# Performance work log

Hardware: AMD Instinct MI355X
Metric: run time of the kernel (lower is better)

The kernel has to match this reference:

```python
import jax, jax.numpy as jnp
import numpy as np

UNITS = 1024      # LSTM hidden size
FEAT = 128        # num_features (Dense output == cell input for feedback)
T = 48            # warmup sequence length
B = 2048          # batch
OUT_STEPS = 24
S0, S1 = 0, 128   # output_indices[0] : output_indices[-1]+1


def setup_inputs() -> dict:
    key = jax.random.key(0)
    k0, k1, k2, k3 = jax.random.split(key, 4)
    inputs = jax.random.normal(k0, (B, T, FEAT), dtype=jnp.float32)
    # Keras LSTMCell params: kernel [F,4U], recurrent_kernel [U,4U], bias [4U] (gate order i,f,c,o)
    kernel = jax.random.normal(k1, (FEAT, 4 * UNITS), dtype=jnp.float32) * 0.05
    recurrent_kernel = jax.random.normal(k2, (UNITS, 4 * UNITS), dtype=jnp.float32) * 0.02
    bias = jnp.zeros((4 * UNITS,), dtype=jnp.float32)
    dense_w = jax.random.normal(k3, (UNITS, FEAT), dtype=jnp.float32) * 0.03
    dense_b = jnp.zeros((FEAT,), dtype=jnp.float32)
    return {"inputs": inputs, "kernel": kernel, "recurrent_kernel": recurrent_kernel,
            "bias": bias, "dense_w": dense_w, "dense_b": dense_b}


def _lstm_step(h, c, x, kernel, recurrent_kernel, bias):
    # Keras LSTMCell: z = x@W + h@U + b, gates split as (i, f, g, o)
    z = x @ kernel + h @ recurrent_kernel + bias
    i, f, g, o = jnp.split(z, 4, axis=-1)
    i = jax.nn.sigmoid(i)
    f = jax.nn.sigmoid(f)
    g = jnp.tanh(g)
    o = jax.nn.sigmoid(o)
    c_new = f * c + i * g
    h_new = o * jnp.tanh(c_new)
    return h_new, c_new


def reference(inputs, kernel, recurrent_kernel, bias, dense_w, dense_b):
    bsz = inputs.shape[0]
    h0 = jnp.zeros((bsz, UNITS), dtype=inputs.dtype)
    c0 = jnp.zeros((bsz, UNITS), dtype=inputs.dtype)

    # warmup: RNN over the input sequence, keep final state
    def warm_step(carry, x_t):
        h, c = carry
        h, c = _lstm_step(h, c, x_t, kernel, recurrent_kernel, bias)
        return (h, c), None

    (h, c), _ = jax.lax.scan(warm_step, (h0, c0), jnp.swapaxes(inputs, 0, 1))  # xs: [T,B,F]
    y = h @ dense_w + dense_b  # first prediction, [B, F]

    def dec_step(carry, _):
        h, c, y_prev = carry
        h, c = _lstm_step(h, c, y_prev, kernel, recurrent_kernel, bias)
        y_new = h @ dense_w + dense_b
        return (h, c, y_new), y_new[:, S0:S1]

    _, ys_rest = jax.lax.scan(dec_step, (h, c, y), None, length=OUT_STEPS - 1)  # [OUT-1,B,S]
    ys = jnp.concatenate([y[None, :, S0:S1], ys_rest], axis=0)  # [OUT,B,S]
    return jnp.transpose(ys, (1, 0, 2))  # [B, OUT, S]
```

## Files before the change

kernel.cpp:

```cpp
#include <hip/hip_runtime.h>
#include <math.h>

#define UNITS 1024
#define FEAT 128
#define TSEQ 48
#define BATCH 2048
#define OUT_STEPS 24
#define KTOT 1152
#define N4 4096

typedef unsigned short ushort;
typedef __attribute__((ext_vector_type(8))) short bf16x8;
typedef __attribute__((ext_vector_type(4))) float f32x4;

__device__ __forceinline__ ushort f2bf(float f) {
  unsigned u = __float_as_uint(f);
  unsigned r = (u + 0x7FFF + ((u >> 16) & 1)) >> 16;
  return (ushort)r;
}
__device__ __forceinline__ float sigm(float x) { return 1.0f / (1.0f + __expf(-x)); }
__device__ __forceinline__ float tanh_f(float x) { return 1.0f - 2.0f / (1.0f + __expf(2.0f * x)); }

__device__ __forceinline__ void gload_lds16(const void* g, void* l) {
  __builtin_amdgcn_global_load_lds(
      (const __attribute__((address_space(1))) unsigned int*)g,
      (__attribute__((address_space(3))) unsigned int*)l, 16, 0, 0);
}


__global__ __launch_bounds__(256)
void convert_inputs_kernel(const float* __restrict__ in, ushort* __restrict__ Xb) {
  const int o4 = (blockIdx.x * 256 + threadIdx.x) * 4;
  const int t = o4 >> 18;
  const int b = (o4 >> 7) & 2047;
  const int f = o4 & 127;
  const float4 v = *reinterpret_cast<const float4*>(&in[(size_t)(b * TSEQ + t) * FEAT + f]);
  union { ushort u[4]; unsigned long long ll; } w;
  w.u[0] = f2bf(v.x); w.u[1] = f2bf(v.y); w.u[2] = f2bf(v.z); w.u[3] = f2bf(v.w);
  *reinterpret_cast<unsigned long long*>(&Xb[o4]) = w.ll;
}

__global__ __launch_bounds__(256)
void prep_w_kernel(const float* __restrict__ kW, const float* __restrict__ rW,
                   ushort* __restrict__ Wp) {
  __shared__ ushort tile[32][65];
  const int t = threadIdx.x;
  const int k0 = blockIdx.x * 32;
  const int n0 = blockIdx.y * 64;
#pragma unroll
  for (int p = 0; p < 8; ++p) {
    const int li = p * 256 + t;
    const int nn = li & 63, kk = li >> 6;
    const int np = n0 + nn;
    const int u16 = np & 15, gg = (np >> 4) & 3, ugrp = np >> 6;
    const int nsrc = gg * 1024 + ugrp * 16 + u16;
    const int k = k0 + kk;
    const float v = (k < FEAT) ? kW[(size_t)k * N4 + nsrc] : rW[(size_t)(k - FEAT) * N4 + nsrc];
    tile[kk][nn] = f2bf(v);
  }
  __syncthreads();
#pragma unroll
  for (int p = 0; p < 8; ++p) {
    const int li = p * 256 + t;
    const int kk = li & 31, nn = li >> 5;
    Wp[(size_t)(n0 + nn) * KTOT + k0 + kk] = tile[kk][nn];
  }
}

__global__ __launch_bounds__(256)
void prep_wd_kernel(const float* __restrict__ dw, ushort* __restrict__ Wdt) {
  const int o = blockIdx.x * 256 + threadIdx.x;
  const int n = o >> 10, k = o & 1023;
  Wdt[o] = f2bf(dw[(size_t)k * FEAT + n]);
}

__global__ __launch_bounds__(256)
void prep_b2_kernel(const float* __restrict__ bias, const float* __restrict__ db,
                    const float* __restrict__ W, float* __restrict__ b2) {
  const int n = blockIdx.x * 256 + threadIdx.x;
  float s = bias[n];
#pragma unroll 8
  for (int f = 0; f < FEAT; ++f) s += db[f] * W[(size_t)f * N4 + n];
  b2[n] = s;
}

__global__ __launch_bounds__(256)
void prep_u_kernel(const float* __restrict__ dw,
                   const float* __restrict__ W,
                   const float* __restrict__ rW,
                   ushort* __restrict__ Wp2) {
  __shared__ float sWd[64][132];
  __shared__ float sW[128][68];
  const int tid = threadIdx.x;
  const int ugrp = blockIdx.x;
  const int k0 = blockIdx.y * 64;
  const int n0 = ugrp * 64;

#pragma unroll
  for (int p = 0; p < 8; ++p) {
    const int li = p * 256 + tid;
    const int kk = li >> 5, f4 = (li & 31) * 4;
    *reinterpret_cast<float4*>(&sWd[kk][f4]) =
        *reinterpret_cast<const float4*>(&dw[(size_t)(k0 + kk) * FEAT + f4]);
  }
#pragma unroll
  for (int p = 0; p < 32; ++p) {
    const int li = p * 256 + tid;
    const int f = li >> 6, nn = li & 63;
    const int u16 = nn & 15, gg = (nn >> 4) & 3;
    const int nsrc = gg * 1024 + ugrp * 16 + u16;
    sW[f][nn] = W[(size_t)f * N4 + nsrc];
  }
  __syncthreads();

  const int tx = tid & 15;
  const int ty = tid >> 4;
  float acc[4][4] = {};
  for (int f = 0; f < 128; ++f) {
    float a[4], b[4];
#pragma unroll
    for (int j = 0; j < 4; ++j) a[j] = sWd[tx * 4 + j][f];
#pragma unroll
    for (int i = 0; i < 4; ++i) b[i] = sW[f][ty * 4 + i];
#pragma unroll
    for (int i = 0; i < 4; ++i)
#pragma unroll
      for (int j = 0; j < 4; ++j) acc[i][j] += a[j] * b[i];
  }

#pragma unroll
  for (int i = 0; i < 4; ++i) {
    const int np = n0 + ty * 4 + i;
    const int u16 = np & 15, gg = (np >> 4) & 3;
    const int nsrc = gg * 1024 + ugrp * 16 + u16;
#pragma unroll
    for (int j = 0; j < 4; ++j) {
      const int k = k0 + tx * 4 + j;
      const float v = rW[(size_t)k * N4 + nsrc] + acc[i][j];
      Wp2[(size_t)np * UNITS + k] = f2bf(v);
    }
  }
}

template<int KT, bool HASX>
__global__ __launch_bounds__(512, 4)
void lstm_step_kernel(const ushort* __restrict__ Xc,
                      const ushort* __restrict__ Hin,
                      const ushort* __restrict__ Wp,
                      const float* __restrict__ bias,
                      float* __restrict__ C,
                      ushort* __restrict__ Hout) {
  __shared__ alignas(16) ushort sA[2][128 * 32];
  __shared__ alignas(16) ushort sB[2][128 * 32];

  const int bid = blockIdx.x;
  const int wg = (bid & 7) * 64 + (bid >> 3);
  const int bx = wg & 15, by = wg >> 4;
  const int bm = bx * 128;
  const int bn = by * 128;

  const int tid = threadIdx.x;
  const int wid = tid >> 6;
  const int l = tid & 63;
  const int wr = wid >> 1;
  const int wc = wid & 1;

  const int rloc = l >> 2;
  const int slot = l & 3;
  const int gsw = slot ^ ((rloc >> 1) & 3);
  const int l15 = l & 15;
  const int kg = l >> 4;

  f32x4 acc[2][4] = {};

  auto STAGE = [&](int k0s, int bsel) {
#pragma unroll
    for (int q = 0; q < 2; ++q) {
      const int c = wid * 2 + q;
      if (c < 8) {
        const int r = c * 16 + rloc;
        const ushort* src;
        if (HASX && k0s < FEAT)
          src = Xc + (size_t)(bm + r) * FEAT + k0s + gsw * 8;
        else
          src = Hin + (size_t)(bm + r) * UNITS + (k0s - (HASX ? FEAT : 0)) + gsw * 8;
        gload_lds16(src, &sA[bsel][c * 512]);
      } else {
        const int cb = c - 8;
        const int r = cb * 16 + rloc;
        const ushort* src = Wp + (size_t)(bn + r) * KT + k0s + gsw * 8;
        gload_lds16(src, &sB[bsel][cb * 512]);
      }
    }
  };

  constexpr int NT = KT / 32;
  STAGE(0, 0);
  __syncthreads();
  int cur = 0;
  for (int t = 0; t < NT; ++t) {
    if (t + 1 < NT) STAGE((t + 1) * 32, cur ^ 1);

    bf16x8 av[2], bv[4];
#pragma unroll
    for (int m = 0; m < 2; ++m) {
      const int r = wr * 32 + m * 16 + l15;
      const int sph = kg ^ ((r >> 1) & 3);
      av[m] = *reinterpret_cast<const bf16x8*>(&sA[cur][r * 32 + sph * 8]);
    }
#pragma unroll
    for (int n = 0; n < 4; ++n) {
      const int r = wc * 64 + n * 16 + l15;
      const int sph = kg ^ ((r >> 1) & 3);
      bv[n] = *reinterpret_cast<const bf16x8*>(&sB[cur][r * 32 + sph * 8]);
    }
#pragma unroll
    for (int m = 0; m < 2; ++m)
#pragma unroll
      for (int n = 0; n < 4; ++n)
        acc[m][n] = __builtin_amdgcn_mfma_f32_16x16x32_bf16(av[m], bv[n], acc[m][n], 0, 0, 0);

    __syncthreads();
    cur ^= 1;
  }

  const int unit = (by * 2 + wc) * 16 + l15;
  const float bi = bias[unit];
  const float bf_ = bias[1024 + unit];
  const float bg = bias[2048 + unit];
  const float bo = bias[3072 + unit];

#pragma unroll
  for (int m = 0; m < 2; ++m) {
    const int rowb = bm + wr * 32 + m * 16 + kg * 4;
#pragma unroll
    for (int j = 0; j < 4; ++j) {
      const size_t a = (size_t)(rowb + j) * UNITS + unit;
      const float i_ = sigm(acc[m][0][j] + bi);
      const float f_ = sigm(acc[m][1][j] + bf_);
      const float g_ = tanh_f(acc[m][2][j] + bg);
      const float o_ = sigm(acc[m][3][j] + bo);
      const float cn = f_ * C[a] + i_ * g_;
      C[a] = cn;
      Hout[a] = f2bf(o_ * tanh_f(cn));
    }
  }
}

__global__ __launch_bounds__(256)
void dense_all_kernel(const ushort* __restrict__ Hall,
                      const ushort* __restrict__ Wdt,
                      const float* __restrict__ db,
                      float* __restrict__ out) {
  __shared__ alignas(16) ushort sA[2][64 * 32];
  __shared__ alignas(16) ushort sB[2][128 * 32];

  const int bm = blockIdx.x * 64;
  const int tid = threadIdx.x;
  const int wid = tid >> 6;
  const int l = tid & 63;
  const int wr = wid >> 1;
  const int wc = wid & 1;

  const int rloc = l >> 2;
  const int slot = l & 3;
  const int gsw = slot ^ ((rloc >> 1) & 3);
  const int l15 = l & 15;
  const int kg = l >> 4;

  f32x4 acc[2][4] = {};

  auto STAGE = [&](int k0s, int bsel) {
#pragma unroll
    for (int q = 0; q < 3; ++q) {
      const int c = wid * 3 + q;
      if (c < 4) {
        const int r = c * 16 + rloc;
        gload_lds16(Hall + (size_t)(bm + r) * UNITS + k0s + gsw * 8, &sA[bsel][c * 512]);
      } else {
        const int cb = c - 4;
        const int r = cb * 16 + rloc;
        gload_lds16(Wdt + (size_t)r * UNITS + k0s + gsw * 8, &sB[bsel][cb * 512]);
      }
    }
  };

  STAGE(0, 0);
  __syncthreads();
  int cur = 0;
  for (int t = 0; t < 32; ++t) {
    if (t + 1 < 32) STAGE((t + 1) * 32, cur ^ 1);

    bf16x8 av[2], bv[4];
#pragma unroll
    for (int m = 0; m < 2; ++m) {
      const int r = wr * 32 + m * 16 + l15;
      const int sph = kg ^ ((r >> 1) & 3);
      av[m] = *reinterpret_cast<const bf16x8*>(&sA[cur][r * 32 + sph * 8]);
    }
#pragma unroll
    for (int n = 0; n < 4; ++n) {
      const int r = wc * 64 + n * 16 + l15;
      const int sph = kg ^ ((r >> 1) & 3);
      bv[n] = *reinterpret_cast<const bf16x8*>(&sB[cur][r * 32 + sph * 8]);
    }
#pragma unroll
    for (int m = 0; m < 2; ++m)
#pragma unroll
      for (int n = 0; n < 4; ++n)
        acc[m][n] = __builtin_amdgcn_mfma_f32_16x16x32_bf16(av[m], bv[n], acc[m][n], 0, 0, 0);

    __syncthreads();
    cur ^= 1;
  }

#pragma unroll
  for (int n = 0; n < 4; ++n) {
    const int f = wc * 64 + n * 16 + l15;
    const float bb = db[f];
#pragma unroll
    for (int m = 0; m < 2; ++m) {
#pragma unroll
      for (int j = 0; j < 4; ++j) {
        const int r = bm + wr * 32 + m * 16 + kg * 4 + j;
        const int s = r >> 11, b = r & 2047;
        out[((size_t)b * OUT_STEPS + s) * FEAT + f] = acc[m][n][j] + bb;
      }
    }
  }
}

extern "C" void kernel_launch(void* const* d_in, const int* in_sizes, int n_in,
                              void* d_out, int out_size, void* d_ws, size_t ws_size,
                              hipStream_t stream) {
  const float* inputs  = (const float*)d_in[0];
  const float* kernelW = (const float*)d_in[1];
  const float* recW    = (const float*)d_in[2];
  const float* bias    = (const float*)d_in[3];
  const float* dw      = (const float*)d_in[4];
  const float* db      = (const float*)d_in[5];
  float* out = (float*)d_out;

  char* ws = (char*)d_ws;
  float* C    = (float*)ws;
  ushort* Xb  = (ushort*)(ws + 8388608);
  ushort* Wp2 = Xb;
  ushort* Hb0 = (ushort*)(ws + 33554432);
  ushort* Hb1 = (ushort*)(ws + 37748736);
  ushort* Wp  = (ushort*)(ws + 41943040);
  ushort* Wdt = (ushort*)(ws + 51380224);
  float*  b2  = (float*)(ws + 51642368);
  ushort* Hall = (ushort*)(ws + 51658752);
  ushort* Hb[2] = {Hb0, Hb1};
  const size_t HSLOT = (size_t)BATCH * UNITS;

  convert_inputs_kernel<<<TSEQ * BATCH * FEAT / 1024, 256, 0, stream>>>(inputs, Xb);
  prep_w_kernel<<<dim3(KTOT / 32, N4 / 64), 256, 0, stream>>>(kernelW, recW, Wp);
  prep_wd_kernel<<<FEAT * UNITS / 256, 256, 0, stream>>>(dw, Wdt);
  prep_b2_kernel<<<N4 / 256, 256, 0, stream>>>(bias, db, kernelW, b2);
  hipMemsetAsync(C, 0, 8388608, stream);
  hipMemsetAsync(Hb0, 0, 4194304, stream);

  int cur = 0;
  for (int t = 0; t < TSEQ; ++t) {
    ushort* hout = (t == TSEQ - 1) ? Hall : Hb[cur ^ 1];
    lstm_step_kernel<KTOT, true><<<512, 512, 0, stream>>>(
        Xb + (size_t)t * BATCH * FEAT, Hb[cur], Wp, bias, C, hout);
    cur ^= 1;
  }
  prep_u_kernel<<<dim3(64, 16), 256, 0, stream>>>(dw, kernelW, recW, Wp2);

  for (int s = 1; s < OUT_STEPS; ++s) {
    lstm_step_kernel<UNITS, false><<<512, 512, 0, stream>>>(
        nullptr, Hall + (size_t)(s - 1) * HSLOT, Wp2, b2, C, Hall + (size_t)s * HSLOT);
  }
  dense_all_kernel<<<(OUT_STEPS * BATCH) / 64, 256, 0, stream>>>(Hall, Wdt, db, out);
}
```

Measured before the change: 2.227 ms.

## Load LSTM weights directly into registers in MFMA fragment layout, skip LDS for B

Weights are pre-packed into the MFMA fragment order so each lane loads its B operand straight from global memory into registers, double-buffered across iterations, while only the hidden-state A tile is staged through LDS with a K step of 64. The block shrinks to 256 threads with a 4x4 MFMA tile per wave, and the cell state is stored in a fragment-native layout and prefetched before the GEMM. The first step skips the zero hidden-state part of the GEMM and the C/H memsets. This removes B tile LDS traffic and some synchronization, at the cost of more register pressure and reliance on hand-written waitcnt counts.

```diff
diff --git a/kernel.cpp b/kernel.cpp
--- a/kernel.cpp
+++ b/kernel.cpp
@@ -41,30 +41,24 @@
 }
 
 __global__ __launch_bounds__(256)
-void prep_w_kernel(const float* __restrict__ kW, const float* __restrict__ rW,
-                   ushort* __restrict__ Wp) {
-  __shared__ ushort tile[32][65];
-  const int t = threadIdx.x;
-  const int k0 = blockIdx.x * 32;
-  const int n0 = blockIdx.y * 64;
-#pragma unroll
-  for (int p = 0; p < 8; ++p) {
-    const int li = p * 256 + t;
-    const int nn = li & 63, kk = li >> 6;
-    const int np = n0 + nn;
-    const int u16 = np & 15, gg = (np >> 4) & 3, ugrp = np >> 6;
-    const int nsrc = gg * 1024 + ugrp * 16 + u16;
-    const int k = k0 + kk;
-    const float v = (k < FEAT) ? kW[(size_t)k * N4 + nsrc] : rW[(size_t)(k - FEAT) * N4 + nsrc];
-    tile[kk][nn] = f2bf(v);
-  }
-  __syncthreads();
-#pragma unroll
-  for (int p = 0; p < 8; ++p) {
-    const int li = p * 256 + t;
-    const int kk = li & 31, nn = li >> 5;
-    Wp[(size_t)(n0 + nn) * KTOT + k0 + kk] = tile[kk][nn];
-  }
+void prep_wF_kernel(const float* __restrict__ kW, const float* __restrict__ rW,
+                    ushort* __restrict__ WpF) {
+  const int g = blockIdx.x * 256 + threadIdx.x;
+  const int lane = g & 63;
+  const int kc = (g >> 6) % 36;
+  const int cf = g / 2304;
+  const int np = cf * 16 + (lane & 15);
+  const int kbase = kc * 32 + (lane >> 4) * 8;
+  const int u16 = np & 15, gg = (np >> 4) & 3, ugrp = np >> 6;
+  const int nsrc = gg * 1024 + ugrp * 16 + u16;
+  ushort v[8];
+#pragma unroll
+  for (int e = 0; e < 8; ++e) {
+    const int k = kbase + e;
+    const float f = (k < FEAT) ? kW[(size_t)k * N4 + nsrc] : rW[(size_t)(k - FEAT) * N4 + nsrc];
+    v[e] = f2bf(f);
+  }
+  *reinterpret_cast<bf16x8*>(&WpF[(size_t)g * 8]) = *reinterpret_cast<bf16x8*>(v);
 }
 
 __global__ __launch_bounds__(256)
@@ -88,7 +82,7 @@
 void prep_u_kernel(const float* __restrict__ dw,
                    const float* __restrict__ W,
                    const float* __restrict__ rW,
-                   ushort* __restrict__ Wp2) {
+                   ushort* __restrict__ Wp2F) {
   __shared__ float sWd[64][132];
   __shared__ float sW[128][68];
   const int tid = threadIdx.x;
@@ -133,31 +127,32 @@
     const int np = n0 + ty * 4 + i;
     const int u16 = np & 15, gg = (np >> 4) & 3;
     const int nsrc = gg * 1024 + ugrp * 16 + u16;
+    const int cf = np >> 4;
 #pragma unroll
     for (int j = 0; j < 4; ++j) {
       const int k = k0 + tx * 4 + j;
       const float v = rW[(size_t)k * N4 + nsrc] + acc[i][j];
-      Wp2[(size_t)np * UNITS + k] = f2bf(v);
-    }
-  }
-}
-
-template<int KT, bool HASX>
-__global__ __launch_bounds__(512, 4)
+      const int kc = k >> 5, lane = ((k >> 3) & 3) * 16 + (np & 15), e = k & 7;
+      Wp2F[(((size_t)cf * 32 + kc) * 64 + lane) * 8 + e] = f2bf(v);
+    }
+  }
+}
+
+template<int KT, int NKS, bool HASX, bool ZC>
+__global__ __launch_bounds__(256, 2)
 void lstm_step_kernel(const ushort* __restrict__ Xc,
                       const ushort* __restrict__ Hin,
-                      const ushort* __restrict__ Wp,
+                      const ushort* __restrict__ WpF,
                       const float* __restrict__ bias,
-                      float* __restrict__ C,
+                      float* __restrict__ CF,
                       ushort* __restrict__ Hout) {
-  __shared__ alignas(16) ushort sA[2][128 * 32];
-  __shared__ alignas(16) ushort sB[2][128 * 32];
+  __shared__ alignas(16) ushort sA[2 * 8192];
 
   const int bid = blockIdx.x;
   const int wg = (bid & 7) * 64 + (bid >> 3);
   const int bx = wg & 15, by = wg >> 4;
   const int bm = bx * 128;
-  const int bn = by * 128;
+  const int bnf = by * 8;
 
   const int tid = threadIdx.x;
   const int wid = tid >> 6;
@@ -170,80 +165,115 @@
   const int gsw = slot ^ ((rloc >> 1) & 3);
   const int l15 = l & 15;
   const int kg = l >> 4;
-
-  f32x4 acc[2][4] = {};
-
-  auto STAGE = [&](int k0s, int bsel) {
-#pragma unroll
-    for (int q = 0; q < 2; ++q) {
-      const int c = wid * 2 + q;
-      if (c < 8) {
-        const int r = c * 16 + rloc;
-        const ushort* src;
-        if (HASX && k0s < FEAT)
-          src = Xc + (size_t)(bm + r) * FEAT + k0s + gsw * 8;
-        else
-          src = Hin + (size_t)(bm + r) * UNITS + (k0s - (HASX ? FEAT : 0)) + gsw * 8;
-        gload_lds16(src, &sA[bsel][c * 512]);
-      } else {
-        const int cb = c - 8;
-        const int r = cb * 16 + rloc;
-        const ushort* src = Wp + (size_t)(bn + r) * KT + k0s + gsw * 8;
-        gload_lds16(src, &sB[bsel][cb * 512]);
+  const int nfbase = bnf + wc * 4;
+
+  constexpr int NT = KT / 64;
+
+  f32x4 acc[4][4] = {};
+  bf16x8 bv0[2][4], bv1[2][4];
+
+  const int R = bx * 2 + wr;
+  const int U = by * 2 + wc;
+  const size_t cfbase = (((size_t)R * 64 + U) * 64 + l) * 16;
+  f32x4 cpre[4];
+  if (!ZC) {
+#pragma unroll
+    for (int m = 0; m < 4; ++m)
+      cpre[m] = *reinterpret_cast<const f32x4*>(CF + cfbase + m * 4);
+  }
+
+  auto STAGE_A = [&](int t) {
+    const int bufofs = (t & 1) * 8192;
+    const int k0base = t * 64;
+#pragma unroll
+    for (int q = 0; q < 4; ++q) {
+      const int c = wid * 4 + q;
+      const int r = (c & 7) * 16 + rloc;
+      const int k0s = k0base + (c >> 3) * 32;
+      const ushort* src;
+      if (HASX && k0s < FEAT) src = Xc + (size_t)(bm + r) * FEAT + k0s + gsw * 8;
+      else                    src = Hin + (size_t)(bm + r) * UNITS + (k0s - (HASX ? FEAT : 0)) + gsw * 8;
+      gload_lds16(src, &sA[bufofs + c * 512]);
+    }
+  };
+
+  auto LOADB = [&](int t, bf16x8 (&bv)[2][4]) {
+#pragma unroll
+    for (int kk = 0; kk < 2; ++kk)
+#pragma unroll
+      for (int n = 0; n < 4; ++n) {
+        const size_t kc = (size_t)(t * 2 + kk);
+        bv[kk][n] = *reinterpret_cast<const bf16x8*>(
+            WpF + (((size_t)(nfbase + n) * NKS + kc) * 64 + l) * 8);
       }
-    }
   };
 
-  constexpr int NT = KT / 32;
-  STAGE(0, 0);
-  __syncthreads();
-  int cur = 0;
-  for (int t = 0; t < NT; ++t) {
-    if (t + 1 < NT) STAGE((t + 1) * 32, cur ^ 1);
-
-    bf16x8 av[2], bv[4];
-#pragma unroll
-    for (int m = 0; m < 2; ++m) {
-      const int r = wr * 32 + m * 16 + l15;
-      const int sph = kg ^ ((r >> 1) & 3);
-      av[m] = *reinterpret_cast<const bf16x8*>(&sA[cur][r * 32 + sph * 8]);
-    }
-#pragma unroll
-    for (int n = 0; n < 4; ++n) {
-      const int r = wc * 64 + n * 16 + l15;
-      const int sph = kg ^ ((r >> 1) & 3);
-      bv[n] = *reinterpret_cast<const bf16x8*>(&sB[cur][r * 32 + sph * 8]);
-    }
-#pragma unroll
-    for (int m = 0; m < 2; ++m)
-#pragma unroll
-      for (int n = 0; n < 4; ++n)
-        acc[m][n] = __builtin_amdgcn_mfma_f32_16x16x32_bf16(av[m], bv[n], acc[m][n], 0, 0, 0);
-
-    __syncthreads();
-    cur ^= 1;
-  }
-
-  const int unit = (by * 2 + wc) * 16 + l15;
+  auto COMPUTE = [&](int t, bf16x8 (&bv)[2][4]) {
+    const int bufofs = (t & 1) * 8192;
+    bf16x8 av[2][4];
+#pragma unroll
+    for (int kk = 0; kk < 2; ++kk)
+#pragma unroll
+      for (int m = 0; m < 4; ++m) {
+        const int r = wr * 64 + m * 16 + l15;
+        const int sph = kg ^ ((r >> 1) & 3);
+        av[kk][m] = *reinterpret_cast<const bf16x8*>(&sA[bufofs + kk * 4096 + r * 32 + sph * 8]);
+      }
+    __builtin_amdgcn_s_setprio(1);
+#pragma unroll
+    for (int kk = 0; kk < 2; ++kk)
+#pragma unroll
+      for (int m = 0; m < 4; ++m)
+#pragma unroll
+        for (int n = 0; n < 4; ++n)
+          acc[m][n] = __builtin_amdgcn_mfma_f32_16x16x32_bf16(av[kk][m], bv[kk][n], acc[m][n], 0, 0, 0);
+    __builtin_amdgcn_s_setprio(0);
+  };
+
+  auto ITER = [&](int t, bf16x8 (&bvU)[2][4], bf16x8 (&bvL)[2][4], bool last) {
+    if (!last) {
+      STAGE_A(t + 1);
+      LOADB(t + 1, bvL);
+    }
+    __builtin_amdgcn_sched_barrier(0);
+    if (!last) asm volatile("s_waitcnt vmcnt(12)" ::: "memory");
+    else       asm volatile("s_waitcnt vmcnt(0)" ::: "memory");
+    asm volatile("s_barrier" ::: "memory");
+    COMPUTE(t, bvU);
+    asm volatile("s_barrier" ::: "memory");
+  };
+
+  STAGE_A(0);
+  LOADB(0, bv0);
+
+  for (int tp = 0; tp < (NT - 2) / 2; ++tp) {
+    ITER(2 * tp, bv0, bv1, false);
+    ITER(2 * tp + 1, bv1, bv0, false);
+  }
+  ITER(NT - 2, bv0, bv1, false);
+  ITER(NT - 1, bv1, bv0, true);
+
+  const int unit = U * 16 + l15;
   const float bi = bias[unit];
   const float bf_ = bias[1024 + unit];
   const float bg = bias[2048 + unit];
   const float bo = bias[3072 + unit];
 
 #pragma unroll
-  for (int m = 0; m < 2; ++m) {
-    const int rowb = bm + wr * 32 + m * 16 + kg * 4;
+  for (int m = 0; m < 4; ++m) {
+    const int rowb = bm + wr * 64 + m * 16 + kg * 4;
+    f32x4 cout;
 #pragma unroll
     for (int j = 0; j < 4; ++j) {
-      const size_t a = (size_t)(rowb + j) * UNITS + unit;
       const float i_ = sigm(acc[m][0][j] + bi);
       const float f_ = sigm(acc[m][1][j] + bf_);
       const float g_ = tanh_f(acc[m][2][j] + bg);
       const float o_ = sigm(acc[m][3][j] + bo);
-      const float cn = f_ * C[a] + i_ * g_;
-      C[a] = cn;
-      Hout[a] = f2bf(o_ * tanh_f(cn));
-    }
+      const float cn = ZC ? (i_ * g_) : (f_ * cpre[m][j] + i_ * g_);
+      cout[j] = cn;
+      Hout[(size_t)(rowb + j) * UNITS + unit] = f2bf(o_ * tanh_f(cn));
+    }
+    *reinterpret_cast<f32x4*>(CF + cfbase + m * 4) = cout;
   }
 }
 
@@ -342,37 +372,37 @@
   float* out = (float*)d_out;
 
   char* ws = (char*)d_ws;
-  float* C    = (float*)ws;
-  ushort* Xb  = (ushort*)(ws + 8388608);
-  ushort* Wp2 = Xb;
-  ushort* Hb0 = (ushort*)(ws + 33554432);
-  ushort* Hb1 = (ushort*)(ws + 37748736);
-  ushort* Wp  = (ushort*)(ws + 41943040);
-  ushort* Wdt = (ushort*)(ws + 51380224);
-  float*  b2  = (float*)(ws + 51642368);
+  float*  CF   = (float*)ws;
+  ushort* Xb   = (ushort*)(ws + 8388608);
+  ushort* Wp2F = Xb;
+  ushort* Hb0  = (ushort*)(ws + 33554432);
+  ushort* Hb1  = (ushort*)(ws + 37748736);
+  ushort* WpF  = (ushort*)(ws + 41943040);
+  ushort* Wdt  = (ushort*)(ws + 51380224);
+  float*  b2   = (float*)(ws + 51642368);
   ushort* Hall = (ushort*)(ws + 51658752);
   ushort* Hb[2] = {Hb0, Hb1};
   const size_t HSLOT = (size_t)BATCH * UNITS;
 
   convert_inputs_kernel<<<TSEQ * BATCH * FEAT / 1024, 256, 0, stream>>>(inputs, Xb);
-  prep_w_kernel<<<dim3(KTOT / 32, N4 / 64), 256, 0, stream>>>(kernelW, recW, Wp);
+  prep_wF_kernel<<<(N4 / 16) * 36 * 64 / 256, 256, 0, stream>>>(kernelW, recW, WpF);
   prep_wd_kernel<<<FEAT * UNITS / 256, 256, 0, stream>>>(dw, Wdt);
   prep_b2_kernel<<<N4 / 256, 256, 0, stream>>>(bias, db, kernelW, b2);
-  hipMemsetAsync(C, 0, 8388608, stream);
-  hipMemsetAsync(Hb0, 0, 4194304, stream);
-
-  int cur = 0;
-  for (int t = 0; t < TSEQ; ++t) {
+
+  lstm_step_kernel<128, 36, true, true><<<512, 256, 0, stream>>>(
+      Xb, Hb0 , WpF, bias, CF, Hb1);
+  int cur = 1;
+  for (int t = 1; t < TSEQ; ++t) {
     ushort* hout = (t == TSEQ - 1) ? Hall : Hb[cur ^ 1];
-    lstm_step_kernel<KTOT, true><<<512, 512, 0, stream>>>(
-        Xb + (size_t)t * BATCH * FEAT, Hb[cur], Wp, bias, C, hout);
+    lstm_step_kernel<KTOT, 36, true, false><<<512, 256, 0, stream>>>(
+        Xb + (size_t)t * BATCH * FEAT, Hb[cur], WpF, bias, CF, hout);
     cur ^= 1;
   }
-  prep_u_kernel<<<dim3(64, 16), 256, 0, stream>>>(dw, kernelW, recW, Wp2);
+  prep_u_kernel<<<dim3(64, 16), 256, 0, stream>>>(dw, kernelW, recW, Wp2F);
 
   for (int s = 1; s < OUT_STEPS; ++s) {
-    lstm_step_kernel<UNITS, false><<<512, 512, 0, stream>>>(
-        nullptr, Hall + (size_t)(s - 1) * HSLOT, Wp2, b2, C, Hall + (size_t)s * HSLOT);
+    lstm_step_kernel<UNITS, 32, false, false><<<512, 256, 0, stream>>>(
+        nullptr, Hall + (size_t)(s - 1) * HSLOT, Wp2F, b2, CF, Hall + (size_t)s * HSLOT);
   }
   dense_all_kernel<<<(OUT_STEPS * BATCH) / 64, 256, 0, stream>>>(Hall, Wdt, db, out);
 }
```

New measurement: 2.003 ms. -10.1%, faster.
